# Performance work log

Measured on AMD Instinct MI355X. Metric: run time of the kernel, lower is better.

## Reference

```python
import jax, jax.numpy as jnp
import numpy as np

N_NODES = 200000
MAX_DEG = 128
S1, S2 = 25, 10  # neighbor sample sizes per hop (GraphSAGE defaults)


def setup_inputs() -> dict:
    key = jax.random.key(0)
    ks = jax.random.split(key, 9)
    F, H, C, B = 256, 128, 41, 1024
    return {
        "node_ids": jax.random.randint(ks[0], (B,), 0, N_NODES, dtype=jnp.int32),
        "features": jax.random.normal(ks[1], (N_NODES, F), dtype=jnp.float32),
        "adj_info": jax.random.randint(ks[2], (N_NODES, MAX_DEG), 0, N_NODES, dtype=jnp.int32),
        "W_self1": jax.random.normal(ks[3], (F, H), dtype=jnp.float32) * 0.05,
        "W_neigh1": jax.random.normal(ks[4], (F, H), dtype=jnp.float32) * 0.05,
        "W_self2": jax.random.normal(ks[5], (2 * H, H), dtype=jnp.float32) * 0.05,
        "W_neigh2": jax.random.normal(ks[6], (2 * H, H), dtype=jnp.float32) * 0.05,
        "W_pred": jax.random.normal(ks[7], (2 * H, C), dtype=jnp.float32) * 0.05,
        "b_pred": jnp.zeros((C,), dtype=jnp.float32),
    }


def _sample(adj_info, node_ids):
    """Uniform neighbor sampling: hop1 [B,S1], hop2 [B,S1,S2]."""
    k1, k2 = jax.random.split(jax.random.key(42))
    B = node_ids.shape[0]
    cols1 = jax.random.randint(k1, (B, S1), 0, MAX_DEG)
    hop1 = jnp.take_along_axis(adj_info[node_ids], cols1, axis=1)  # [B,S1]
    cols2 = jax.random.randint(k2, (B * S1, S2), 0, MAX_DEG)
    hop2 = jnp.take_along_axis(adj_info[hop1.reshape(-1)], cols2, axis=1)
    return hop1, hop2.reshape(B, S1, S2)


def _mean_agg(self_f, neigh_f, Ws, Wn, act):
    # GraphSAGE MeanAggregator with concat: [self@Ws ; mean(neigh)@Wn]
    neigh = neigh_f.mean(axis=-2)
    return act(jnp.concatenate([self_f @ Ws, neigh @ Wn], axis=-1))


def reference(node_ids, features, adj_info, W_self1, W_neigh1, W_self2, W_neigh2, W_pred, b_pred):
    hop1, hop2 = _sample(adj_info, node_ids)
    f0 = features[node_ids]      # [B,F]
    f1 = features[hop1]          # [B,S1,F]
    f2 = features[hop2]          # [B,S1,S2,F]

    h0 = _mean_agg(f0, f1, W_self1, W_neigh1, jax.nn.relu)   # [B,2H]
    h1 = _mean_agg(f1, f2, W_self1, W_neigh1, jax.nn.relu)   # [B,S1,2H]
    h = _mean_agg(h0, h1, W_self2, W_neigh2, lambda x: x)    # [B,2H]

    # tf.math.l2_normalize(x, 1): x * rsqrt(max(sum(x^2), 1e-12))
    h = h * jax.lax.rsqrt(jnp.maximum(jnp.sum(h * h, axis=1, keepdims=True), 1e-12))
    logits = h @ W_pred + b_pred
    return jax.nn.softmax(logits, axis=-1)
```

## Files before the change

kernel.cpp:

```cpp
#include <hip/hip_runtime.h>
#include <cstdint>
#include <cstddef>

#define BATCH 1024
#define S1 25
#define S2 10
#define FDIM 256
#define HDIM 128
#define NCLS 41
#define MAXDEG 128

typedef __attribute__((ext_vector_type(8))) short bf16x8;
typedef __attribute__((ext_vector_type(4))) float f32x4;

__host__ __device__ static inline void tf2x32(uint32_t k0, uint32_t k1,
                                              uint32_t c0, uint32_t c1,
                                              uint32_t& o0, uint32_t& o1) {
  const uint32_t ks2 = k0 ^ k1 ^ 0x1BD11BDAu;
  uint32_t x0 = c0 + k0, x1 = c1 + k1;
#define TFR(r) { x0 += x1; x1 = (x1 << (r)) | (x1 >> (32 - (r))); x1 ^= x0; }
  TFR(13) TFR(15) TFR(26) TFR(6)
  x0 += k1;  x1 += ks2 + 1u;
  TFR(17) TFR(29) TFR(16) TFR(24)
  x0 += ks2; x1 += k0 + 2u;
  TFR(13) TFR(15) TFR(26) TFR(6)
  x0 += k0;  x1 += k1 + 3u;
  TFR(17) TFR(29) TFR(16) TFR(24)
  x0 += k1;  x1 += ks2 + 4u;
  TFR(13) TFR(15) TFR(26) TFR(6)
  x0 += ks2; x1 += k0 + 5u;
#undef TFR
  o0 = x0; o1 = x1;
}

__device__ static inline uint32_t rand_bits_at(uint32_t kb0, uint32_t kb1, uint32_t j) {
  uint32_t o0, o1;
  tf2x32(kb0, kb1, 0u, j, o0, o1);
  return o0 ^ o1;
}

__device__ static inline ushort f2bf(float x) {
  uint32_t u = __float_as_uint(x);
  return (ushort)((u + 0x7fffu + ((u >> 16) & 1u)) >> 16);
}

__global__ __launch_bounds__(256)
void prep_kernel(const int* __restrict__ node_ids, const float* __restrict__ feat,
                 const int* __restrict__ adj,
                 const float* __restrict__ Ws1, const float* __restrict__ Wn1,
                 ushort* __restrict__ n2m, float* __restrict__ n1m,
                 ushort* __restrict__ f1b, ushort* __restrict__ WbT,
                 float* __restrict__ h1m,
                 uint32_t kb1_0, uint32_t kb1_1, uint32_t kb2_0, uint32_t kb2_1) {
  const int blk = blockIdx.x;
  const int t = threadIdx.x;
  if (blk < 6400) {
    const int wave = t >> 6, lane = t & 63;
    const int g = blk * 4 + wave;
    const int b = g / S1;
    int hop1v = 0;
    if (lane == 0) {
      uint32_t c1 = rand_bits_at(kb1_0, kb1_1, (uint32_t)g) & (MAXDEG - 1);
      hop1v = adj[(size_t)node_ids[b] * MAXDEG + c1];
    }
    hop1v = __shfl(hop1v, 0, 64);
    int r2id = 0;
    if (lane < S2) {
      uint32_t c2 = rand_bits_at(kb2_0, kb2_1, (uint32_t)(g * S2 + lane)) & (MAXDEG - 1);
      r2id = adj[(size_t)hop1v * MAXDEG + c2];
    }
    float4 acc = make_float4(0.f, 0.f, 0.f, 0.f);
#pragma unroll
    for (int r = 0; r < S2; ++r) {
      int rid = __shfl(r2id, r, 64);
      float4 v = ((const float4*)(feat + (size_t)rid * FDIM))[lane];
      acc.x += v.x; acc.y += v.y; acc.z += v.z; acc.w += v.w;
    }
    const float inv = 1.f / S2;
    ushort4 o;
    o.x = f2bf(acc.x * inv); o.y = f2bf(acc.y * inv);
    o.z = f2bf(acc.z * inv); o.w = f2bf(acc.w * inv);
    *(ushort4*)(n2m + (size_t)g * FDIM + lane * 4) = o;
  } else if (blk < 6656) {
    const int wave = t >> 6, lane = t & 63;
    const int b = (blk - 6400) * 4 + wave;
    int h1v = 0;
    if (lane < S1) {
      uint32_t c1 = rand_bits_at(kb1_0, kb1_1, (uint32_t)(b * S1 + lane)) & (MAXDEG - 1);
      h1v = adj[(size_t)node_ids[b] * MAXDEG + c1];
    }
    float4 acc = make_float4(0.f, 0.f, 0.f, 0.f);
#pragma unroll
    for (int r = 0; r < S1; ++r) {
      int rid = __shfl(h1v, r, 64);
      float4 v = ((const float4*)(feat + (size_t)rid * FDIM))[lane];
      acc.x += v.x; acc.y += v.y; acc.z += v.z; acc.w += v.w;
      ushort4 o;
      o.x = f2bf(v.x); o.y = f2bf(v.y); o.z = f2bf(v.z); o.w = f2bf(v.w);
      *(ushort4*)(f1b + (size_t)(b * S1 + r) * FDIM + lane * 4) = o;
    }
    const float inv = 1.f / S1;
    acc.x *= inv; acc.y *= inv; acc.z *= inv; acc.w *= inv;
    ((float4*)(n1m + (size_t)b * FDIM))[lane] = acc;
  } else if (blk < 6912) {
    const int idx = blk - 6656;
    const int h = idx >> 7, n = idx & 127;
    const float* W = h ? Wn1 : Ws1;
    WbT[(size_t)idx * FDIM + t] = f2bf(W[(size_t)t * HDIM + n]);
  } else {
    const int i = (blk - 6912) * 256 + t;
    ((float4*)h1m)[i] = make_float4(0.f, 0.f, 0.f, 0.f);
  }
}

__global__ __launch_bounds__(256, 3)
void mfma_h1_kernel(const ushort* __restrict__ f1b, const ushort* __restrict__ n2m,
                    const ushort* __restrict__ WbT, float* __restrict__ h1m) {
  const int half = blockIdx.y;
  const ushort* Amat = half ? n2m : f1b;
  const ushort* Bmat = WbT + (size_t)half * HDIM * FDIM;
  const int m0 = blockIdx.x * 64;
  const int tid = threadIdx.x;
  const int wave = tid >> 6;
  const int lane = tid & 63;
  const int lq = lane >> 4;
  const int lr = lane & 15;

  __shared__ ushort As[64][40];
  __shared__ ushort Bs[128][40];
  __shared__ float  Cs[64][132];

  f32x4 acc[4][2];
#pragma unroll
  for (int rt = 0; rt < 4; ++rt)
#pragma unroll
    for (int ct = 0; ct < 2; ++ct) acc[rt][ct] = (f32x4)(0.f);

  for (int k0 = 0; k0 < FDIM; k0 += 32) {
    const int row = tid >> 2, kc = (tid & 3) * 8;
    {
      int4 v = *(const int4*)(Amat + (size_t)(m0 + row) * FDIM + k0 + kc);
      *(int4*)&As[row][kc] = v;
    }
#pragma unroll
    for (int i = 0; i < 2; ++i) {
      int idx = tid + i * 256;
      int n = idx >> 2, kc2 = (idx & 3) * 8;
      int4 v = *(const int4*)(Bmat + (size_t)n * FDIM + k0 + kc2);
      *(int4*)&Bs[n][kc2] = v;
    }
    __syncthreads();

    bf16x8 af[4];
#pragma unroll
    for (int rt = 0; rt < 4; ++rt)
      af[rt] = *(const bf16x8*)&As[rt * 16 + lr][lq * 8];
#pragma unroll
    for (int ct = 0; ct < 2; ++ct) {
      bf16x8 bf = *(const bf16x8*)&Bs[wave * 32 + ct * 16 + lr][lq * 8];
#pragma unroll
      for (int rt = 0; rt < 4; ++rt)
        acc[rt][ct] = __builtin_amdgcn_mfma_f32_16x16x32_bf16(af[rt], bf, acc[rt][ct], 0, 0, 0);
    }
    __syncthreads();
  }

#pragma unroll
  for (int rt = 0; rt < 4; ++rt)
#pragma unroll
    for (int ct = 0; ct < 2; ++ct)
#pragma unroll
      for (int r = 0; r < 4; ++r)
        Cs[rt * 16 + lq * 4 + r][wave * 32 + ct * 16 + lr] = fmaxf(acc[rt][ct][r], 0.f);
  __syncthreads();

  if (tid < 128) {
    const int c = tid;
    const int coff = half * HDIM + c;
    float s = 0.f;
    int curb = m0 / S1;
    for (int m = 0; m < 64; ++m) {
      int b = (m0 + m) / S1;
      if (b != curb) {
        atomicAdd(&h1m[(size_t)curb * (2 * HDIM) + coff], s * (1.f / S1));
        s = 0.f; curb = b;
      }
      s += Cs[m][c];
    }
    atomicAdd(&h1m[(size_t)curb * (2 * HDIM) + coff], s * (1.f / S1));
  }
}

__global__ __launch_bounds__(256)
void tail_kernel(const int* __restrict__ node_ids, const float* __restrict__ feat,
                 const float* __restrict__ n1m, const float* __restrict__ h1m,
                 const float* __restrict__ Ws1, const float* __restrict__ Wn1,
                 const float* __restrict__ Ws2, const float* __restrict__ Wn2,
                 const float* __restrict__ Wp, const float* __restrict__ bp,
                 float* __restrict__ out) {
  const int b0 = blockIdx.x * 2;
  const int t = threadIdx.x;
  const int wave = t >> 6, lane = t & 63;

  __shared__ float A0[2][256];
  __shared__ float A1[2][256];
  __shared__ float H1[2][256];
  __shared__ float H0[2][256];
  __shared__ float HN[2][256];
  __shared__ float WpL[2 * HDIM * NCLS];
  __shared__ float bpL[NCLS];
  __shared__ float red[4][2];
  __shared__ float scl[2];
  __shared__ float lg[2][48];
  __shared__ float sm[2][2];

  if (wave < 2) {
    const int r = wave;
    const int nid = node_ids[b0 + r];
    ((float4*)A0[r])[lane] = ((const float4*)(feat + (size_t)nid * FDIM))[lane];
    ((float4*)A1[r])[lane] = ((const float4*)(n1m + (size_t)(b0 + r) * FDIM))[lane];
  } else {
    const int r = wave - 2;
    ((float4*)H1[r])[lane] = ((const float4*)(h1m + (size_t)(b0 + r) * FDIM))[lane];
  }
  for (int i = t; i < (2 * HDIM * NCLS) / 4; i += 256)
    ((float4*)WpL)[i] = ((const float4*)Wp)[i];
  if (t < NCLS) bpL[t] = bp[t];
  __syncthreads();

  const int h = t >> 7, c = t & 127;
  {
    const float* W = h ? Wn1 : Ws1;
    const float* Ap = h ? &A1[0][0] : &A0[0][0];
    float acc0 = 0.f, acc1 = 0.f;
#pragma unroll 4
    for (int k4 = 0; k4 < 64; ++k4) {
      float w0 = W[(size_t)(k4 * 4 + 0) * HDIM + c];
      float w1 = W[(size_t)(k4 * 4 + 1) * HDIM + c];
      float w2 = W[(size_t)(k4 * 4 + 2) * HDIM + c];
      float w3 = W[(size_t)(k4 * 4 + 3) * HDIM + c];
      float4 a0 = ((const float4*)(Ap))[k4];
      float4 a1 = ((const float4*)(Ap + 256))[k4];
      acc0 += a0.x * w0 + a0.y * w1 + a0.z * w2 + a0.w * w3;
      acc1 += a1.x * w0 + a1.y * w1 + a1.z * w2 + a1.w * w3;
    }
    H0[0][t] = fmaxf(acc0, 0.f);
    H0[1][t] = fmaxf(acc1, 0.f);
  }
  __syncthreads();

  float hv0, hv1;
  {
    const float* W = h ? Wn2 : Ws2;
    const float* Ap = h ? &H1[0][0] : &H0[0][0];
    float acc0 = 0.f, acc1 = 0.f;
#pragma unroll 4
    for (int k4 = 0; k4 < 64; ++k4) {
      float w0 = W[(size_t)(k4 * 4 + 0) * HDIM + c];
      float w1 = W[(size_t)(k4 * 4 + 1) * HDIM + c];
      float w2 = W[(size_t)(k4 * 4 + 2) * HDIM + c];
      float w3 = W[(size_t)(k4 * 4 + 3) * HDIM + c];
      float4 a0 = ((const float4*)(Ap))[k4];
      float4 a1 = ((const float4*)(Ap + 256))[k4];
      acc0 += a0.x * w0 + a0.y * w1 + a0.z * w2 + a0.w * w3;
      acc1 += a1.x * w0 + a1.y * w1 + a1.z * w2 + a1.w * w3;
    }
    hv0 = acc0; hv1 = acc1;
  }

  {
    float s0 = hv0 * hv0, s1 = hv1 * hv1;
#pragma unroll
    for (int off = 32; off; off >>= 1) {
      s0 += __shfl_xor(s0, off, 64);
      s1 += __shfl_xor(s1, off, 64);
    }
    if (lane == 0) { red[wave][0] = s0; red[wave][1] = s1; }
  }
  __syncthreads();
  if (t < 2) {
    float tot = red[0][t] + red[1][t] + red[2][t] + red[3][t];
    scl[t] = rsqrtf(fmaxf(tot, 1e-12f));
  }
  __syncthreads();
  HN[0][t] = hv0 * scl[0];
  HN[1][t] = hv1 * scl[1];
  __syncthreads();

  {
    const int g = t >> 2, q = t & 3;
    for (int p = g; p < 2 * NCLS; p += 64) {
      const int rr = (p >= NCLS) ? 1 : 0;
      const int cc = p - rr * NCLS;
      float s = 0.f;
#pragma unroll 8
      for (int k = 0; k < 64; ++k)
        s += HN[rr][q * 64 + k] * WpL[(size_t)(q * 64 + k) * NCLS + cc];
      s += __shfl_xor(s, 1, 64);
      s += __shfl_xor(s, 2, 64);
      if (q == 0) lg[rr][cc] = s + bpL[cc];
    }
  }
  __syncthreads();
  if (t < 2) {
    float m = -1e30f;
    for (int i = 0; i < NCLS; ++i) m = fmaxf(m, lg[t][i]);
    float s = 0.f;
    for (int i = 0; i < NCLS; ++i) s += expf(lg[t][i] - m);
    sm[t][0] = m; sm[t][1] = s;
  }
  __syncthreads();
  if (t < 2 * NCLS) {
    const int rr = (t >= NCLS) ? 1 : 0;
    const int cc = t - rr * NCLS;
    out[(size_t)(b0 + rr) * NCLS + cc] = expf(lg[rr][cc] - sm[rr][0]) / sm[rr][1];
  }
}

extern "C" void kernel_launch(void* const* d_in, const int* in_sizes, int n_in,
                              void* d_out, int out_size, void* d_ws, size_t ws_size,
                              hipStream_t stream) {
  const int*   node_ids = (const int*)d_in[0];
  const float* features = (const float*)d_in[1];
  const int*   adj      = (const int*)d_in[2];
  const float* Ws1      = (const float*)d_in[3];
  const float* Wn1      = (const float*)d_in[4];
  const float* Ws2      = (const float*)d_in[5];
  const float* Wn2      = (const float*)d_in[6];
  const float* Wp       = (const float*)d_in[7];
  const float* bp       = (const float*)d_in[8];
  float* out = (float*)d_out;

  char* ws = (char*)d_ws;
  ushort* n2m  = (ushort*)(ws + 0);
  ushort* f1b  = (ushort*)(ws + 13107200);
  ushort* WbT  = (ushort*)(ws + 26214400);
  float*  n1m  = (float*)(ws + 26345472);
  float*  h1m  = (float*)(ws + 27394048);

  uint32_t k1_0, k1_1, k2_0, k2_1, kb1_0, kb1_1, kb2_0, kb2_1;
  tf2x32(0u, 42u, 0u, 0u, k1_0, k1_1);
  tf2x32(0u, 42u, 0u, 1u, k2_0, k2_1);
  tf2x32(k1_0, k1_1, 0u, 1u, kb1_0, kb1_1);
  tf2x32(k2_0, k2_1, 0u, 1u, kb2_0, kb2_1);

  prep_kernel<<<7168, 256, 0, stream>>>(node_ids, features, adj, Ws1, Wn1,
                                        n2m, n1m, f1b, WbT, h1m,
                                        kb1_0, kb1_1, kb2_0, kb2_1);

  dim3 gBig(BATCH * S1 / 64, 2);
  mfma_h1_kernel<<<gBig, 256, 0, stream>>>(f1b, n2m, WbT, h1m);

  tail_kernel<<<BATCH / 2, 256, 0, stream>>>(node_ids, features, n1m, h1m,
                                             Ws1, Wn1, Ws2, Wn2, Wp, bp, out);
}
```

Before: 381.3 us.

## Fuse sampling, gather, MFMA hop-1 aggregation and tail into one per-node kernel

Replaces the prep, MFMA and tail kernels with a single kernel that runs one block per batch node. Each block samples neighbors, gathers features, builds bf16 tiles in LDS, runs the MFMA for the hop-1 transform with a register-level mean reduction, then does the layer-2, normalisation and softmax tail. This drops the large global intermediates (n2m, f1b, n1m, h1m), the atomics and the zeroing pass. The trade-off is that only 1024 blocks of 256 threads carry the whole gather, so parallelism and latency hiding are lower, and the weights are reloaded per block.

```diff
diff --git a/kernel.cpp b/kernel.cpp
--- a/kernel.cpp
+++ b/kernel.cpp
@@ -45,276 +45,211 @@
 }
 
 __global__ __launch_bounds__(256)
-void prep_kernel(const int* __restrict__ node_ids, const float* __restrict__ feat,
-                 const int* __restrict__ adj,
-                 const float* __restrict__ Ws1, const float* __restrict__ Wn1,
-                 ushort* __restrict__ n2m, float* __restrict__ n1m,
-                 ushort* __restrict__ f1b, ushort* __restrict__ WbT,
-                 float* __restrict__ h1m,
-                 uint32_t kb1_0, uint32_t kb1_1, uint32_t kb2_0, uint32_t kb2_1) {
-  const int blk = blockIdx.x;
-  const int t = threadIdx.x;
-  if (blk < 6400) {
-    const int wave = t >> 6, lane = t & 63;
-    const int g = blk * 4 + wave;
-    const int b = g / S1;
-    int hop1v = 0;
-    if (lane == 0) {
-      uint32_t c1 = rand_bits_at(kb1_0, kb1_1, (uint32_t)g) & (MAXDEG - 1);
-      hop1v = adj[(size_t)node_ids[b] * MAXDEG + c1];
-    }
-    hop1v = __shfl(hop1v, 0, 64);
-    int r2id = 0;
-    if (lane < S2) {
-      uint32_t c2 = rand_bits_at(kb2_0, kb2_1, (uint32_t)(g * S2 + lane)) & (MAXDEG - 1);
-      r2id = adj[(size_t)hop1v * MAXDEG + c2];
-    }
-    float4 acc = make_float4(0.f, 0.f, 0.f, 0.f);
-#pragma unroll
-    for (int r = 0; r < S2; ++r) {
-      int rid = __shfl(r2id, r, 64);
-      float4 v = ((const float4*)(feat + (size_t)rid * FDIM))[lane];
-      acc.x += v.x; acc.y += v.y; acc.z += v.z; acc.w += v.w;
-    }
-    const float inv = 1.f / S2;
-    ushort4 o;
-    o.x = f2bf(acc.x * inv); o.y = f2bf(acc.y * inv);
-    o.z = f2bf(acc.z * inv); o.w = f2bf(acc.w * inv);
-    *(ushort4*)(n2m + (size_t)g * FDIM + lane * 4) = o;
-  } else if (blk < 6656) {
-    const int wave = t >> 6, lane = t & 63;
-    const int b = (blk - 6400) * 4 + wave;
-    int h1v = 0;
-    if (lane < S1) {
-      uint32_t c1 = rand_bits_at(kb1_0, kb1_1, (uint32_t)(b * S1 + lane)) & (MAXDEG - 1);
-      h1v = adj[(size_t)node_ids[b] * MAXDEG + c1];
-    }
-    float4 acc = make_float4(0.f, 0.f, 0.f, 0.f);
-#pragma unroll
-    for (int r = 0; r < S1; ++r) {
-      int rid = __shfl(h1v, r, 64);
-      float4 v = ((const float4*)(feat + (size_t)rid * FDIM))[lane];
-      acc.x += v.x; acc.y += v.y; acc.z += v.z; acc.w += v.w;
-      ushort4 o;
-      o.x = f2bf(v.x); o.y = f2bf(v.y); o.z = f2bf(v.z); o.w = f2bf(v.w);
-      *(ushort4*)(f1b + (size_t)(b * S1 + r) * FDIM + lane * 4) = o;
-    }
-    const float inv = 1.f / S1;
-    acc.x *= inv; acc.y *= inv; acc.z *= inv; acc.w *= inv;
-    ((float4*)(n1m + (size_t)b * FDIM))[lane] = acc;
-  } else if (blk < 6912) {
-    const int idx = blk - 6656;
-    const int h = idx >> 7, n = idx & 127;
-    const float* W = h ? Wn1 : Ws1;
-    WbT[(size_t)idx * FDIM + t] = f2bf(W[(size_t)t * HDIM + n]);
-  } else {
-    const int i = (blk - 6912) * 256 + t;
-    ((float4*)h1m)[i] = make_float4(0.f, 0.f, 0.f, 0.f);
-  }
+void wprep_kernel(const float* __restrict__ Ws1, const float* __restrict__ Wn1,
+                  ushort* __restrict__ WbT) {
+  const int idx = blockIdx.x;
+  const int h = idx >> 7, n = idx & 127;
+  const float* W = h ? Wn1 : Ws1;
+  WbT[(size_t)idx * FDIM + threadIdx.x] = f2bf(W[(size_t)threadIdx.x * HDIM + n]);
 }
 
 __global__ __launch_bounds__(256, 3)
-void mfma_h1_kernel(const ushort* __restrict__ f1b, const ushort* __restrict__ n2m,
-                    const ushort* __restrict__ WbT, float* __restrict__ h1m) {
-  const int half = blockIdx.y;
-  const ushort* Amat = half ? n2m : f1b;
-  const ushort* Bmat = WbT + (size_t)half * HDIM * FDIM;
-  const int m0 = blockIdx.x * 64;
-  const int tid = threadIdx.x;
-  const int wave = tid >> 6;
-  const int lane = tid & 63;
-  const int lq = lane >> 4;
-  const int lr = lane & 15;
-
-  __shared__ ushort As[64][40];
-  __shared__ ushort Bs[128][40];
-  __shared__ float  Cs[64][132];
-
-  f32x4 acc[4][2];
-#pragma unroll
-  for (int rt = 0; rt < 4; ++rt)
-#pragma unroll
-    for (int ct = 0; ct < 2; ++ct) acc[rt][ct] = (f32x4)(0.f);
-
-  for (int k0 = 0; k0 < FDIM; k0 += 32) {
-    const int row = tid >> 2, kc = (tid & 3) * 8;
-    {
-      int4 v = *(const int4*)(Amat + (size_t)(m0 + row) * FDIM + k0 + kc);
-      *(int4*)&As[row][kc] = v;
-    }
-#pragma unroll
-    for (int i = 0; i < 2; ++i) {
-      int idx = tid + i * 256;
-      int n = idx >> 2, kc2 = (idx & 3) * 8;
-      int4 v = *(const int4*)(Bmat + (size_t)n * FDIM + k0 + kc2);
-      *(int4*)&Bs[n][kc2] = v;
-    }
-    __syncthreads();
-
-    bf16x8 af[4];
-#pragma unroll
-    for (int rt = 0; rt < 4; ++rt)
-      af[rt] = *(const bf16x8*)&As[rt * 16 + lr][lq * 8];
-#pragma unroll
-    for (int ct = 0; ct < 2; ++ct) {
-      bf16x8 bf = *(const bf16x8*)&Bs[wave * 32 + ct * 16 + lr][lq * 8];
-#pragma unroll
-      for (int rt = 0; rt < 4; ++rt)
-        acc[rt][ct] = __builtin_amdgcn_mfma_f32_16x16x32_bf16(af[rt], bf, acc[rt][ct], 0, 0, 0);
-    }
-    __syncthreads();
-  }
-
-#pragma unroll
-  for (int rt = 0; rt < 4; ++rt)
-#pragma unroll
-    for (int ct = 0; ct < 2; ++ct)
-#pragma unroll
-      for (int r = 0; r < 4; ++r)
-        Cs[rt * 16 + lq * 4 + r][wave * 32 + ct * 16 + lr] = fmaxf(acc[rt][ct][r], 0.f);
-  __syncthreads();
-
-  if (tid < 128) {
-    const int c = tid;
-    const int coff = half * HDIM + c;
-    float s = 0.f;
-    int curb = m0 / S1;
-    for (int m = 0; m < 64; ++m) {
-      int b = (m0 + m) / S1;
-      if (b != curb) {
-        atomicAdd(&h1m[(size_t)curb * (2 * HDIM) + coff], s * (1.f / S1));
-        s = 0.f; curb = b;
-      }
-      s += Cs[m][c];
-    }
-    atomicAdd(&h1m[(size_t)curb * (2 * HDIM) + coff], s * (1.f / S1));
-  }
-}
-
-__global__ __launch_bounds__(256)
-void tail_kernel(const int* __restrict__ node_ids, const float* __restrict__ feat,
-                 const float* __restrict__ n1m, const float* __restrict__ h1m,
+void mega_kernel(const int* __restrict__ node_ids, const float* __restrict__ feat,
+                 const int* __restrict__ adj, const ushort* __restrict__ WbT,
                  const float* __restrict__ Ws1, const float* __restrict__ Wn1,
                  const float* __restrict__ Ws2, const float* __restrict__ Wn2,
                  const float* __restrict__ Wp, const float* __restrict__ bp,
-                 float* __restrict__ out) {
-  const int b0 = blockIdx.x * 2;
+                 float* __restrict__ out,
+                 uint32_t kb1_0, uint32_t kb1_1, uint32_t kb2_0, uint32_t kb2_1) {
+  const int b = blockIdx.x;
   const int t = threadIdx.x;
   const int wave = t >> 6, lane = t & 63;
-
-  __shared__ float A0[2][256];
-  __shared__ float A1[2][256];
-  __shared__ float H1[2][256];
-  __shared__ float H0[2][256];
-  __shared__ float HN[2][256];
-  __shared__ float WpL[2 * HDIM * NCLS];
-  __shared__ float bpL[NCLS];
-  __shared__ float red[4][2];
-  __shared__ float scl[2];
-  __shared__ float lg[2][48];
-  __shared__ float sm[2][2];
-
-  if (wave < 2) {
-    const int r = wave;
-    const int nid = node_ids[b0 + r];
-    ((float4*)A0[r])[lane] = ((const float4*)(feat + (size_t)nid * FDIM))[lane];
-    ((float4*)A1[r])[lane] = ((const float4*)(n1m + (size_t)(b0 + r) * FDIM))[lane];
-  } else {
-    const int r = wave - 2;
-    ((float4*)H1[r])[lane] = ((const float4*)(h1m + (size_t)(b0 + r) * FDIM))[lane];
-  }
-  for (int i = t; i < (2 * HDIM * NCLS) / 4; i += 256)
-    ((float4*)WpL)[i] = ((const float4*)Wp)[i];
-  if (t < NCLS) bpL[t] = bp[t];
-  __syncthreads();
-
-  const int h = t >> 7, c = t & 127;
-  {
-    const float* W = h ? Wn1 : Ws1;
-    const float* Ap = h ? &A1[0][0] : &A0[0][0];
-    float acc0 = 0.f, acc1 = 0.f;
+  const int lq = lane >> 4, lr = lane & 15;
+
+  __shared__ int    hop1s[S1];
+  __shared__ int    hop2s[S1 * S2];
+  __shared__ ushort As0[8][32][40];
+  __shared__ ushort As1[8][32][40];
+  __shared__ float  F0[FDIM];
+  __shared__ float  N1[4][FDIM];
+  __shared__ float  H1M[2 * HDIM];
+  __shared__ float  H0[2 * HDIM];
+  __shared__ float  HN[2 * HDIM];
+  __shared__ float  red[4];
+  __shared__ float  lg[NCLS];
+  __shared__ float  smx[2];
+
+  const int nid = node_ids[b];
+
+  if (t < S1) {
+    uint32_t c1 = rand_bits_at(kb1_0, kb1_1, (uint32_t)(b * S1 + t)) & (MAXDEG - 1);
+    hop1s[t] = adj[(size_t)nid * MAXDEG + c1];
+  }
+  __syncthreads();
+
+  if (t < S1 * S2) {
+    const int s1 = t / S2, j = t - s1 * S2;
+    uint32_t c2 = rand_bits_at(kb2_0, kb2_1, (uint32_t)((b * S1 + s1) * S2 + j)) & (MAXDEG - 1);
+    hop2s[t] = adj[(size_t)hop1s[s1] * MAXDEG + c2];
+  }
+  if (t < 64) ((float4*)F0)[t] = ((const float4*)(feat + (size_t)nid * FDIM))[t];
+  {
+    ushort4 z; z.x = 0; z.y = 0; z.z = 0; z.w = 0;
+    for (int i = t; i < 448; i += 256) {
+      const int rc = i >> 3, q = i & 7;
+      const int r = 25 + (rc >> 3), ch = rc & 7;
+      *(ushort4*)&As0[ch][r][q * 4] = z;
+      *(ushort4*)&As1[ch][r][q * 4] = z;
+    }
+  }
+  __syncthreads();
+
+  {
+    float ax = 0.f, ay = 0.f, az = 0.f, aw = 0.f;
+    for (int s1 = wave; s1 < S1; s1 += 4) {
+      const int rid1 = hop1s[s1];
+      float4 v = ((const float4*)(feat + (size_t)rid1 * FDIM))[lane];
+      float bx = 0.f, by = 0.f, bz = 0.f, bw = 0.f;
+#pragma unroll
+      for (int r = 0; r < S2; ++r) {
+        const int rid = hop2s[s1 * S2 + r];
+        float4 w = ((const float4*)(feat + (size_t)rid * FDIM))[lane];
+        bx += w.x; by += w.y; bz += w.z; bw += w.w;
+      }
+      ax += v.x; ay += v.y; az += v.z; aw += v.w;
+      ushort4 o1;
+      o1.x = f2bf(v.x); o1.y = f2bf(v.y); o1.z = f2bf(v.z); o1.w = f2bf(v.w);
+      *(ushort4*)&As0[lane >> 3][s1][(lane & 7) * 4] = o1;
+      const float inv2 = 1.f / S2;
+      ushort4 o2;
+      o2.x = f2bf(bx * inv2); o2.y = f2bf(by * inv2);
+      o2.z = f2bf(bz * inv2); o2.w = f2bf(bw * inv2);
+      *(ushort4*)&As1[lane >> 3][s1][(lane & 7) * 4] = o2;
+    }
+    float4 p; p.x = ax; p.y = ay; p.z = az; p.w = aw;
+    ((float4*)N1[wave])[lane] = p;
+  }
+  __syncthreads();
+
+  {
+    const float s = N1[0][t] + N1[1][t] + N1[2][t] + N1[3][t];
+    N1[0][t] = s * (1.f / S1);
+  }
+
+#pragma unroll 1
+  for (int half = 0; half < 2; ++half) {
+    const ushort* Bmat = WbT + (size_t)half * HDIM * FDIM;
+    const ushort (*As)[32][40] = half ? As1 : As0;
+
+    bf16x8 bfr[2][8];
+#pragma unroll
+    for (int ct = 0; ct < 2; ++ct)
+#pragma unroll
+      for (int k0 = 0; k0 < 8; ++k0)
+        bfr[ct][k0] = *(const bf16x8*)(Bmat + (size_t)(wave * 32 + ct * 16 + lr) * FDIM
+                                       + k0 * 32 + lq * 8);
+
+    f32x4 acc[2][2];
+#pragma unroll
+    for (int rt = 0; rt < 2; ++rt)
+#pragma unroll
+      for (int ct = 0; ct < 2; ++ct) acc[rt][ct] = (f32x4)(0.f);
+
+#pragma unroll
+    for (int k0 = 0; k0 < 8; ++k0) {
+      bf16x8 af0 = *(const bf16x8*)&As[k0][lr][lq * 8];
+      bf16x8 af1 = *(const bf16x8*)&As[k0][16 + lr][lq * 8];
+#pragma unroll
+      for (int ct = 0; ct < 2; ++ct) {
+        acc[0][ct] = __builtin_amdgcn_mfma_f32_16x16x32_bf16(af0, bfr[ct][k0], acc[0][ct], 0, 0, 0);
+        acc[1][ct] = __builtin_amdgcn_mfma_f32_16x16x32_bf16(af1, bfr[ct][k0], acc[1][ct], 0, 0, 0);
+      }
+    }
+
+#pragma unroll
+    for (int ct = 0; ct < 2; ++ct) {
+      float s = 0.f;
+#pragma unroll
+      for (int rt = 0; rt < 2; ++rt)
+#pragma unroll
+        for (int r = 0; r < 4; ++r)
+          s += fmaxf(acc[rt][ct][r], 0.f);
+      s += __shfl_xor(s, 16, 64);
+      s += __shfl_xor(s, 32, 64);
+      if (lq == 0) H1M[half * HDIM + wave * 32 + ct * 16 + lr] = s * (1.f / S1);
+    }
+  }
+  __syncthreads();
+
+  const int hh = t >> 7, c = t & 127;
+  {
+    const float* W = hh ? Wn1 : Ws1;
+    const float* Ap = hh ? N1[0] : F0;
+    float acc = 0.f;
 #pragma unroll 4
     for (int k4 = 0; k4 < 64; ++k4) {
-      float w0 = W[(size_t)(k4 * 4 + 0) * HDIM + c];
-      float w1 = W[(size_t)(k4 * 4 + 1) * HDIM + c];
-      float w2 = W[(size_t)(k4 * 4 + 2) * HDIM + c];
-      float w3 = W[(size_t)(k4 * 4 + 3) * HDIM + c];
-      float4 a0 = ((const float4*)(Ap))[k4];
-      float4 a1 = ((const float4*)(Ap + 256))[k4];
-      acc0 += a0.x * w0 + a0.y * w1 + a0.z * w2 + a0.w * w3;
-      acc1 += a1.x * w0 + a1.y * w1 + a1.z * w2 + a1.w * w3;
-    }
-    H0[0][t] = fmaxf(acc0, 0.f);
-    H0[1][t] = fmaxf(acc1, 0.f);
-  }
-  __syncthreads();
-
-  float hv0, hv1;
-  {
-    const float* W = h ? Wn2 : Ws2;
-    const float* Ap = h ? &H1[0][0] : &H0[0][0];
-    float acc0 = 0.f, acc1 = 0.f;
+      float4 a = ((const float4*)Ap)[k4];
+      acc += a.x * W[(size_t)(k4 * 4 + 0) * HDIM + c]
+           + a.y * W[(size_t)(k4 * 4 + 1) * HDIM + c]
+           + a.z * W[(size_t)(k4 * 4 + 2) * HDIM + c]
+           + a.w * W[(size_t)(k4 * 4 + 3) * HDIM + c];
+    }
+    H0[t] = fmaxf(acc, 0.f);
+  }
+  __syncthreads();
+
+  float hv;
+  {
+    const float* W = hh ? Wn2 : Ws2;
+    const float* Ap = hh ? H1M : H0;
+    float acc = 0.f;
 #pragma unroll 4
     for (int k4 = 0; k4 < 64; ++k4) {
-      float w0 = W[(size_t)(k4 * 4 + 0) * HDIM + c];
-      float w1 = W[(size_t)(k4 * 4 + 1) * HDIM + c];
-      float w2 = W[(size_t)(k4 * 4 + 2) * HDIM + c];
-      float w3 = W[(size_t)(k4 * 4 + 3) * HDIM + c];
-      float4 a0 = ((const float4*)(Ap))[k4];
-      float4 a1 = ((const float4*)(Ap + 256))[k4];
-      acc0 += a0.x * w0 + a0.y * w1 + a0.z * w2 + a0.w * w3;
-      acc1 += a1.x * w0 + a1.y * w1 + a1.z * w2 + a1.w * w3;
-    }
-    hv0 = acc0; hv1 = acc1;
-  }
-
-  {
-    float s0 = hv0 * hv0, s1 = hv1 * hv1;
-#pragma unroll
-    for (int off = 32; off; off >>= 1) {
-      s0 += __shfl_xor(s0, off, 64);
-      s1 += __shfl_xor(s1, off, 64);
-    }
-    if (lane == 0) { red[wave][0] = s0; red[wave][1] = s1; }
-  }
-  __syncthreads();
-  if (t < 2) {
-    float tot = red[0][t] + red[1][t] + red[2][t] + red[3][t];
-    scl[t] = rsqrtf(fmaxf(tot, 1e-12f));
-  }
-  __syncthreads();
-  HN[0][t] = hv0 * scl[0];
-  HN[1][t] = hv1 * scl[1];
+      float4 a = ((const float4*)Ap)[k4];
+      acc += a.x * W[(size_t)(k4 * 4 + 0) * HDIM + c]
+           + a.y * W[(size_t)(k4 * 4 + 1) * HDIM + c]
+           + a.z * W[(size_t)(k4 * 4 + 2) * HDIM + c]
+           + a.w * W[(size_t)(k4 * 4 + 3) * HDIM + c];
+    }
+    hv = acc;
+  }
+
+  {
+    float s = hv * hv;
+#pragma unroll
+    for (int off = 32; off; off >>= 1) s += __shfl_xor(s, off, 64);
+    if (lane == 0) red[wave] = s;
+  }
+  __syncthreads();
+  {
+    const float scl = rsqrtf(fmaxf(red[0] + red[1] + red[2] + red[3], 1e-12f));
+    HN[t] = hv * scl;
+  }
   __syncthreads();
 
   {
     const int g = t >> 2, q = t & 3;
-    for (int p = g; p < 2 * NCLS; p += 64) {
-      const int rr = (p >= NCLS) ? 1 : 0;
-      const int cc = p - rr * NCLS;
+    if (g < NCLS) {
       float s = 0.f;
 #pragma unroll 8
       for (int k = 0; k < 64; ++k)
-        s += HN[rr][q * 64 + k] * WpL[(size_t)(q * 64 + k) * NCLS + cc];
+        s += HN[q * 64 + k] * Wp[(size_t)(q * 64 + k) * NCLS + g];
       s += __shfl_xor(s, 1, 64);
       s += __shfl_xor(s, 2, 64);
-      if (q == 0) lg[rr][cc] = s + bpL[cc];
-    }
-  }
-  __syncthreads();
-  if (t < 2) {
+      if (q == 0) lg[g] = s + bp[g];
+    }
+  }
+  __syncthreads();
+  if (t == 0) {
     float m = -1e30f;
-    for (int i = 0; i < NCLS; ++i) m = fmaxf(m, lg[t][i]);
-    float s = 0.f;
-    for (int i = 0; i < NCLS; ++i) s += expf(lg[t][i] - m);
-    sm[t][0] = m; sm[t][1] = s;
-  }
-  __syncthreads();
-  if (t < 2 * NCLS) {
-    const int rr = (t >= NCLS) ? 1 : 0;
-    const int cc = t - rr * NCLS;
-    out[(size_t)(b0 + rr) * NCLS + cc] = expf(lg[rr][cc] - sm[rr][0]) / sm[rr][1];
-  }
+    for (int i = 0; i < NCLS; ++i) m = fmaxf(m, lg[i]);
+    float ssum = 0.f;
+    for (int i = 0; i < NCLS; ++i) ssum += expf(lg[i] - m);
+    smx[0] = m; smx[1] = ssum;
+  }
+  __syncthreads();
+  if (t < NCLS)
+    out[(size_t)b * NCLS + t] = expf(lg[t] - smx[0]) / smx[1];
 }
 
 extern "C" void kernel_launch(void* const* d_in, const int* in_sizes, int n_in,
@@ -331,12 +266,7 @@
   const float* bp       = (const float*)d_in[8];
   float* out = (float*)d_out;
 
-  char* ws = (char*)d_ws;
-  ushort* n2m  = (ushort*)(ws + 0);
-  ushort* f1b  = (ushort*)(ws + 13107200);
-  ushort* WbT  = (ushort*)(ws + 26214400);
-  float*  n1m  = (float*)(ws + 26345472);
-  float*  h1m  = (float*)(ws + 27394048);
+  ushort* WbT = (ushort*)d_ws;
 
   uint32_t k1_0, k1_1, k2_0, k2_1, kb1_0, kb1_1, kb2_0, kb2_1;
   tf2x32(0u, 42u, 0u, 0u, k1_0, k1_1);
@@ -344,13 +274,9 @@
   tf2x32(k1_0, k1_1, 0u, 1u, kb1_0, kb1_1);
   tf2x32(k2_0, k2_1, 0u, 1u, kb2_0, kb2_1);
 
-  prep_kernel<<<7168, 256, 0, stream>>>(node_ids, features, adj, Ws1, Wn1,
-                                        n2m, n1m, f1b, WbT, h1m,
-                                        kb1_0, kb1_1, kb2_0, kb2_1);
-
-  dim3 gBig(BATCH * S1 / 64, 2);
-  mfma_h1_kernel<<<gBig, 256, 0, stream>>>(f1b, n2m, WbT, h1m);
-
-  tail_kernel<<<BATCH / 2, 256, 0, stream>>>(node_ids, features, n1m, h1m,
-                                             Ws1, Wn1, Ws2, Wn2, Wp, bp, out);
-}
+  wprep_kernel<<<256, 256, 0, stream>>>(Ws1, Wn1, WbT);
+
+  mega_kernel<<<BATCH, 256, 0, stream>>>(node_ids, features, adj, WbT,
+                                         Ws1, Wn1, Ws2, Wn2, Wp, bp, out,
+                                         kb1_0, kb1_1, kb2_0, kb2_1);
+}
```

New measurement: 380.2 us. About the same (-0.3%).
